# Kernel tuning notes

Measured on AMD Instinct MI355X. Metric: run time of the kernel, lower is better.

The kernel has to match this reference:

```python
import jax, jax.numpy as jnp
import numpy as np

B = 256
NE = 19          # electrodes (nodes per graph)
E = 60           # edges per graph
T = 25           # time samples averaged away
EPS = 1e-5


def _bn_channel(x, g, b, rm, rv):
    # x: (B, 19, F); BatchNorm1d over channel dim=1 (eval mode, running stats)
    inv = jax.lax.rsqrt(rv + EPS)
    return (x - rm[None, :, None]) * (g * inv)[None, :, None] + b[None, :, None]


def _bn_feat(x, g, b, rm, rv):
    # x: (N, F); BatchNorm1d over feature dim (eval mode)
    inv = jax.lax.rsqrt(rv + EPS)
    return (x - rm) * (g * inv) + b


def _graph_conv(x, src, dst, ew_rep, w_rel, b_rel, w_root, n_nodes):
    # PyG GraphConv: out_i = W_rel @ sum_{j->i} e_ji * x_j + b_rel + W_root @ x_i
    msg = x[src] * ew_rep[:, None]                         # gather + scale
    agg = jax.ops.segment_sum(msg, dst, num_segments=n_nodes)  # scatter-add
    return agg @ w_rel.T + b_rel + x @ w_root.T


def setup_inputs() -> dict:
    key = jax.random.key(0)
    ks = jax.random.split(key, 24)
    rng = np.random.RandomState(0)
    # base graph: 60 directed edges among 19 nodes
    base = rng.randint(0, NE, size=(2, E)).astype(np.int64)
    offs = (np.arange(B, dtype=np.int64) * NE)[None, :, None]  # (1,B,1)
    ei = (base[:, None, :] + offs).reshape(2, B * E)
    inp = {
        "x": jax.random.normal(ks[0], (B * NE, 40 * 20 * T), dtype=jnp.float32),
        "edge_index": jnp.asarray(ei),
        "batch": jnp.repeat(jnp.arange(B, dtype=jnp.int64), NE),
        "lin2_w": jax.random.normal(ks[1], (256, 800), jnp.float32) * 0.02,
        "lin2_b": jnp.zeros((256,), jnp.float32),
        "bn3_g": jnp.ones((NE,), jnp.float32), "bn3_b": jnp.zeros((NE,), jnp.float32),
        "bn3_rm": jnp.zeros((NE,), jnp.float32), "bn3_rv": jnp.ones((NE,), jnp.float32),
        "lin3_w": jax.random.normal(ks[2], (128, 256), jnp.float32) * 0.02,
        "lin3_b": jnp.zeros((128,), jnp.float32),
        "bn4_g": jnp.ones((NE,), jnp.float32), "bn4_b": jnp.zeros((NE,), jnp.float32),
        "bn4_rm": jnp.zeros((NE,), jnp.float32), "bn4_rv": jnp.ones((NE,), jnp.float32),
        "lin4_w": jax.random.normal(ks[3], (64, 128), jnp.float32) * 0.02,
        "lin4_b": jnp.zeros((64,), jnp.float32),
        "bn5_g": jnp.ones((NE,), jnp.float32), "bn5_b": jnp.zeros((NE,), jnp.float32),
        "bn5_rm": jnp.zeros((NE,), jnp.float32), "bn5_rv": jnp.ones((NE,), jnp.float32),
        "ew1": jnp.ones((E,), jnp.float32),
        "gc1_wrel": jax.random.normal(ks[4], (32, 64), jnp.float32) * 0.1,
        "gc1_brel": jnp.zeros((32,), jnp.float32),
        "gc1_wroot": jax.random.normal(ks[5], (32, 64), jnp.float32) * 0.1,
        "bn6_g": jnp.ones((32,), jnp.float32), "bn6_b": jnp.zeros((32,), jnp.float32),
        "bn6_rm": jnp.zeros((32,), jnp.float32), "bn6_rv": jnp.ones((32,), jnp.float32),
        "ew2": jnp.ones((E,), jnp.float32),
        "gc2_wrel": jax.random.normal(ks[6], (32, 32), jnp.float32) * 0.1,
        "gc2_brel": jnp.zeros((32,), jnp.float32),
        "gc2_wroot": jax.random.normal(ks[7], (32, 32), jnp.float32) * 0.1,
        "bn7_g": jnp.ones((32,), jnp.float32), "bn7_b": jnp.zeros((32,), jnp.float32),
        "bn7_rm": jnp.zeros((32,), jnp.float32), "bn7_rv": jnp.ones((32,), jnp.float32),
        "lin5_w": jax.random.normal(ks[8], (32, 32), jnp.float32) * 0.1,
        "lin5_b": jnp.zeros((32,), jnp.float32),
        "hm_w": jax.random.normal(ks[9], (3, 32), jnp.float32) * 0.1,
        "hm_b": jnp.zeros((3,), jnp.float32),
        "hb_w": jax.random.normal(ks[10], (2, 32), jnp.float32) * 0.1,
        "hb_b": jnp.zeros((2,), jnp.float32),
        "hd_w": jax.random.normal(ks[11], (2, 32), jnp.float32) * 0.1,
        "hd_b": jnp.zeros((2,), jnp.float32),
    }
    return inp


def reference(x, edge_index, batch,
              lin2_w, lin2_b, bn3_g, bn3_b, bn3_rm, bn3_rv,
              lin3_w, lin3_b, bn4_g, bn4_b, bn4_rm, bn4_rv,
              lin4_w, lin4_b, bn5_g, bn5_b, bn5_rm, bn5_rv,
              ew1, gc1_wrel, gc1_brel, gc1_wroot, bn6_g, bn6_b, bn6_rm, bn6_rv,
              ew2, gc2_wrel, gc2_brel, gc2_wroot, bn7_g, bn7_b, bn7_rm, bn7_rv,
              lin5_w, lin5_b, hm_w, hm_b, hb_w, hb_b, hd_w, hd_b):
    n_nodes = x.shape[0]
    b = n_nodes // NE
    # time-average CWT: (B,19,40,20,T) -> (B,19,800)
    h = x.reshape(b, NE, 40, 20, -1).mean(axis=4).reshape(b, NE, 800)
    # dense encoder (dropout = identity in eval)
    h = _bn_channel(jax.nn.relu(h @ lin2_w.T + lin2_b), bn3_g, bn3_b, bn3_rm, bn3_rv)
    h = _bn_channel(jax.nn.relu(h @ lin3_w.T + lin3_b), bn4_g, bn4_b, bn4_rm, bn4_rv)
    h = _bn_channel(jax.nn.relu(h @ lin4_w.T + lin4_b), bn5_g, bn5_b, bn5_rm, bn5_rv)
    h = h.reshape(n_nodes, 64)
    src, dst = edge_index[0], edge_index[1]
    ew1_rep = jnp.tile(ew1, b)
    ew2_rep = jnp.tile(ew2, b)
    h = _graph_conv(h, src, dst, ew1_rep, gc1_wrel, gc1_brel, gc1_wroot, n_nodes)
    h = _bn_feat(jax.nn.relu(h), bn6_g, bn6_b, bn6_rm, bn6_rv)
    h = _graph_conv(h, src, dst, ew2_rep, gc2_wrel, gc2_brel, gc2_wroot, n_nodes)
    h = _bn_feat(jax.nn.relu(h), bn7_g, bn7_b, bn7_rm, bn7_rv)
    # global max pool over nodes of each graph
    z = jax.ops.segment_max(h, batch, num_segments=b)
    z = jax.nn.relu(z @ lin5_w.T + lin5_b)
    return (z @ hm_w.T + hm_b, z @ hb_w.T + hb_b, z @ hd_w.T + hd_b)
```

## Files before the change

kernel.cpp:

```cpp
#include <hip/hip_runtime.h>
#include <math.h>

#define EPSBN 1e-5f

__global__ __launch_bounds__(256)
void mean25_kernel(const float* __restrict__ x, float* __restrict__ h1)
{
    __shared__ __align__(16) float s[6400];
    const int t = threadIdx.x;
    const float4* xv = (const float4*)(x + (size_t)blockIdx.x * 6400);
    float4* sv = (float4*)s;
#pragma unroll
    for (int i = 0; i < 6; ++i) sv[i * 256 + t] = xv[i * 256 + t];
    if (t < 64) sv[1536 + t] = xv[1536 + t];
    __syncthreads();
    const float* p = s + t * 25;
    float acc = 0.f;
#pragma unroll
    for (int k = 0; k < 25; ++k) acc += p[k];
    h1[(size_t)blockIdx.x * 256 + t] = acc * (1.0f / 25.0f);
}

__global__ __launch_bounds__(256)
void sgemm_relu_bnch(const float* __restrict__ A, const float* __restrict__ W,
                     const float* __restrict__ bias,
                     const float* __restrict__ bg, const float* __restrict__ bb,
                     const float* __restrict__ brm, const float* __restrict__ brv,
                     float* __restrict__ C, int M, int N, int K)
{
    __shared__ __align__(16) float As[32][68];
    __shared__ __align__(16) float Ws[32][68];
    const int tid = threadIdx.x;
    const int bm = blockIdx.y * 64;
    const int bn = blockIdx.x * 64;
    const int tm0 = (tid >> 4) * 4;
    const int tn0 = (tid & 15) * 4;
    const int r0 = tid >> 3;
    const int c0 = (tid & 7) * 4;

    float acc[4][4] = {};
    const float* A0 = A + (size_t)(bm + r0) * K + c0;
    const float* A1 = A + (size_t)(bm + r0 + 32) * K + c0;
    const float* W0 = W + (size_t)(bn + r0) * K + c0;
    const float* W1 = W + (size_t)(bn + r0 + 32) * K + c0;

    float4 a0 = *(const float4*)A0;
    float4 a1 = *(const float4*)A1;
    float4 w0 = *(const float4*)W0;
    float4 w1 = *(const float4*)W1;

    for (int k0 = 0; k0 < K; k0 += 32) {
        __syncthreads();
        As[c0 + 0][r0] = a0.x; As[c0 + 1][r0] = a0.y;
        As[c0 + 2][r0] = a0.z; As[c0 + 3][r0] = a0.w;
        As[c0 + 0][r0 + 32] = a1.x; As[c0 + 1][r0 + 32] = a1.y;
        As[c0 + 2][r0 + 32] = a1.z; As[c0 + 3][r0 + 32] = a1.w;
        Ws[c0 + 0][r0] = w0.x; Ws[c0 + 1][r0] = w0.y;
        Ws[c0 + 2][r0] = w0.z; Ws[c0 + 3][r0] = w0.w;
        Ws[c0 + 0][r0 + 32] = w1.x; Ws[c0 + 1][r0 + 32] = w1.y;
        Ws[c0 + 2][r0 + 32] = w1.z; Ws[c0 + 3][r0 + 32] = w1.w;
        __syncthreads();
        if (k0 + 32 < K) {
            a0 = *(const float4*)(A0 + k0 + 32);
            a1 = *(const float4*)(A1 + k0 + 32);
            w0 = *(const float4*)(W0 + k0 + 32);
            w1 = *(const float4*)(W1 + k0 + 32);
        }
#pragma unroll
        for (int kk = 0; kk < 32; ++kk) {
            float4 a = *(const float4*)&As[kk][tm0];
            float4 b = *(const float4*)&Ws[kk][tn0];
            acc[0][0] += a.x * b.x; acc[0][1] += a.x * b.y;
            acc[0][2] += a.x * b.z; acc[0][3] += a.x * b.w;
            acc[1][0] += a.y * b.x; acc[1][1] += a.y * b.y;
            acc[1][2] += a.y * b.z; acc[1][3] += a.y * b.w;
            acc[2][0] += a.z * b.x; acc[2][1] += a.z * b.y;
            acc[2][2] += a.z * b.z; acc[2][3] += a.z * b.w;
            acc[3][0] += a.w * b.x; acc[3][1] += a.w * b.y;
            acc[3][2] += a.w * b.z; acc[3][3] += a.w * b.w;
        }
    }

    const float b0 = bias[bn + tn0 + 0];
    const float b1 = bias[bn + tn0 + 1];
    const float b2 = bias[bn + tn0 + 2];
    const float b3 = bias[bn + tn0 + 3];
#pragma unroll
    for (int i = 0; i < 4; ++i) {
        const int row = bm + tm0 + i;
        const int e = row % 19;
        const float scale = bg[e] * (1.0f / sqrtf(brv[e] + EPSBN));
        const float shift = bb[e] - brm[e] * scale;
        float4 o;
        o.x = fmaxf(acc[i][0] + b0, 0.f) * scale + shift;
        o.y = fmaxf(acc[i][1] + b1, 0.f) * scale + shift;
        o.z = fmaxf(acc[i][2] + b2, 0.f) * scale + shift;
        o.w = fmaxf(acc[i][3] + b3, 0.f) * scale + shift;
        *(float4*)(C + (size_t)row * N + bn + tn0) = o;
    }
}

__global__ __launch_bounds__(256)
void gemm23_fused(const float* __restrict__ h2,
                  const float* __restrict__ w3, const float* __restrict__ b3,
                  const float* __restrict__ g4, const float* __restrict__ bb4,
                  const float* __restrict__ rm4, const float* __restrict__ rv4,
                  const float* __restrict__ w4, const float* __restrict__ b4,
                  const float* __restrict__ g5, const float* __restrict__ bb5,
                  const float* __restrict__ rm5, const float* __restrict__ rv5,
                  float* __restrict__ h4out)
{
    __shared__ __align__(16) float As[32][36];
    __shared__ __align__(16) float Ws[32][132];
    __shared__ __align__(16) float C1[32][132];
    __shared__ __align__(16) float W4T[128][68];

    const int t = threadIdx.x;
    const int bm = blockIdx.x * 32;

    const int tm0 = (t >> 5) * 4;
    const int tn0 = (t & 31) * 4;
    const int ar = t >> 3;
    const int ac = (t & 7) * 4;

    float acc[4][4] = {};
    const float* Ap = h2 + (size_t)(bm + ar) * 256 + ac;
    float4 areg = *(const float4*)Ap;
    float4 wreg[4];
#pragma unroll
    for (int i = 0; i < 4; ++i)
        wreg[i] = *(const float4*)(w3 + (size_t)(ar + i * 32) * 256 + ac);

    for (int k0 = 0; k0 < 256; k0 += 32) {
        __syncthreads();
        As[ac + 0][ar] = areg.x; As[ac + 1][ar] = areg.y;
        As[ac + 2][ar] = areg.z; As[ac + 3][ar] = areg.w;
#pragma unroll
        for (int i = 0; i < 4; ++i) {
            const int row = ar + i * 32;
            Ws[ac + 0][row] = wreg[i].x; Ws[ac + 1][row] = wreg[i].y;
            Ws[ac + 2][row] = wreg[i].z; Ws[ac + 3][row] = wreg[i].w;
        }
        __syncthreads();
        if (k0 + 32 < 256) {
            areg = *(const float4*)(Ap + k0 + 32);
#pragma unroll
            for (int i = 0; i < 4; ++i)
                wreg[i] = *(const float4*)(w3 + (size_t)(ar + i * 32) * 256 + ac + k0 + 32);
        }
#pragma unroll
        for (int kk = 0; kk < 32; ++kk) {
            float4 a = *(const float4*)&As[kk][tm0];
            float4 b = *(const float4*)&Ws[kk][tn0];
            acc[0][0] += a.x * b.x; acc[0][1] += a.x * b.y;
            acc[0][2] += a.x * b.z; acc[0][3] += a.x * b.w;
            acc[1][0] += a.y * b.x; acc[1][1] += a.y * b.y;
            acc[1][2] += a.y * b.z; acc[1][3] += a.y * b.w;
            acc[2][0] += a.z * b.x; acc[2][1] += a.z * b.y;
            acc[2][2] += a.z * b.z; acc[2][3] += a.z * b.w;
            acc[3][0] += a.w * b.x; acc[3][1] += a.w * b.y;
            acc[3][2] += a.w * b.z; acc[3][3] += a.w * b.w;
        }
    }

    {
        const float c0 = b3[tn0 + 0], c1 = b3[tn0 + 1];
        const float c2 = b3[tn0 + 2], c3 = b3[tn0 + 3];
#pragma unroll
        for (int i = 0; i < 4; ++i) {
            const int e = (bm + tm0 + i) % 19;
            const float scale = g4[e] * (1.0f / sqrtf(rv4[e] + EPSBN));
            const float shift = bb4[e] - rm4[e] * scale;
            float4 o;
            o.x = fmaxf(acc[i][0] + c0, 0.f) * scale + shift;
            o.y = fmaxf(acc[i][1] + c1, 0.f) * scale + shift;
            o.z = fmaxf(acc[i][2] + c2, 0.f) * scale + shift;
            o.w = fmaxf(acc[i][3] + c3, 0.f) * scale + shift;
            *(float4*)&C1[tm0 + i][tn0] = o;
        }
    }

    {
        const int ln = t & 63;
        const int wq = t >> 6;
#pragma unroll
        for (int ii = 0; ii < 8; ++ii) {
            const int c4 = wq + ii * 4;
            float4 v = *(const float4*)(w4 + (size_t)ln * 128 + c4 * 4);
            W4T[c4 * 4 + 0][ln] = v.x;
            W4T[c4 * 4 + 1][ln] = v.y;
            W4T[c4 * 4 + 2][ln] = v.z;
            W4T[c4 * 4 + 3][ln] = v.w;
        }
    }
    __syncthreads();

    const int rm2 = (t >> 4) * 2;
    const int cn2 = (t & 15) * 4;
    float acc2[2][4] = {};
#pragma unroll 4
    for (int k = 0; k < 128; ++k) {
        const float a0 = C1[rm2 + 0][k];
        const float a1 = C1[rm2 + 1][k];
        const float4 w = *(const float4*)&W4T[k][cn2];
        acc2[0][0] += a0 * w.x; acc2[0][1] += a0 * w.y;
        acc2[0][2] += a0 * w.z; acc2[0][3] += a0 * w.w;
        acc2[1][0] += a1 * w.x; acc2[1][1] += a1 * w.y;
        acc2[1][2] += a1 * w.z; acc2[1][3] += a1 * w.w;
    }
    {
        const float c0 = b4[cn2 + 0], c1 = b4[cn2 + 1];
        const float c2 = b4[cn2 + 2], c3 = b4[cn2 + 3];
#pragma unroll
        for (int i = 0; i < 2; ++i) {
            const int row = bm + rm2 + i;
            const int e = row % 19;
            const float scale = g5[e] * (1.0f / sqrtf(rv5[e] + EPSBN));
            const float shift = bb5[e] - rm5[e] * scale;
            float4 o;
            o.x = fmaxf(acc2[i][0] + c0, 0.f) * scale + shift;
            o.y = fmaxf(acc2[i][1] + c1, 0.f) * scale + shift;
            o.z = fmaxf(acc2[i][2] + c2, 0.f) * scale + shift;
            o.w = fmaxf(acc2[i][3] + c3, 0.f) * scale + shift;
            *(float4*)(h4out + (size_t)row * 64 + cn2) = o;
        }
    }
}

__global__ __launch_bounds__(128)
void graph_head_kernel(const float* __restrict__ h,
                       const int* __restrict__ ei,
                       const float* __restrict__ ew1, const float* __restrict__ ew2,
                       const float* __restrict__ wrel1, const float* __restrict__ brel1,
                       const float* __restrict__ wroot1,
                       const float* __restrict__ g6, const float* __restrict__ b6,
                       const float* __restrict__ rm6, const float* __restrict__ rv6,
                       const float* __restrict__ wrel2, const float* __restrict__ brel2,
                       const float* __restrict__ wroot2,
                       const float* __restrict__ g7, const float* __restrict__ b7,
                       const float* __restrict__ rm7, const float* __restrict__ rv7,
                       const float* __restrict__ lin5w, const float* __restrict__ lin5b,
                       const float* __restrict__ hmw, const float* __restrict__ hmb,
                       const float* __restrict__ hbw, const float* __restrict__ hbb,
                       const float* __restrict__ hdw, const float* __restrict__ hdb,
                       float* __restrict__ out, int nB, int nEdgeTot)
{
    __shared__ __align__(16) float sh[19 * 64];
    __shared__ __align__(16) float sagg[19 * 64];
    __shared__ __align__(16) float sh2[19 * 32];
    __shared__ __align__(16) float sagg2[19 * 32];
    __shared__ __align__(16) float sh3[19 * 32];
    __shared__ __align__(16) float swrel1[32 * 64];
    __shared__ __align__(16) float swroot1[32 * 64];
    __shared__ __align__(16) float swrel2[32 * 32];
    __shared__ __align__(16) float swroot2[32 * 32];
    __shared__ __align__(16) float slin5[32 * 32];
    __shared__ float sz[32], szz[32];
    __shared__ int ssrc[60], sdst[60];
    __shared__ float sew1[60], sew2[60];

    const int t = threadIdx.x;
    const int g = blockIdx.x;

    for (int i = t; i < 19 * 64; i += 128) { sh[i] = h[(size_t)g * 19 * 64 + i]; sagg[i] = 0.f; }
    for (int i = t; i < 19 * 32; i += 128) sagg2[i] = 0.f;
    for (int i = t; i < 2048; i += 128) { swrel1[i] = wrel1[i]; swroot1[i] = wroot1[i]; }
    for (int i = t; i < 1024; i += 128) { swrel2[i] = wrel2[i]; swroot2[i] = wroot2[i]; slin5[i] = lin5w[i]; }
    if (t < 60) {
        ssrc[t] = ei[g * 60 + t] - g * 19;
        sdst[t] = ei[nEdgeTot + g * 60 + t] - g * 19;
        sew1[t] = ew1[t];
        sew2[t] = ew2[t];
    }
    __syncthreads();

    if (t < 64) {
        for (int e = 0; e < 60; ++e)
            sagg[sdst[e] * 64 + t] += sew1[e] * sh[ssrc[e] * 64 + t];
    }
    __syncthreads();

    for (int idx = t; idx < 19 * 32; idx += 128) {
        const int n = idx >> 5, j = idx & 31;
        const float4* ag = (const float4*)&sagg[n * 64];
        const float4* hg = (const float4*)&sh[n * 64];
        const float4* wr = (const float4*)&swrel1[j * 64];
        const float4* wo = (const float4*)&swroot1[j * 64];
        float acc = brel1[j];
#pragma unroll
        for (int k = 0; k < 16; ++k) {
            float4 a = ag[k], w = wr[k], x = hg[k], u = wo[k];
            acc += a.x * w.x + a.y * w.y + a.z * w.z + a.w * w.w;
            acc += x.x * u.x + x.y * u.y + x.z * u.z + x.w * u.w;
        }
        float v = fmaxf(acc, 0.f);
        const float scale = g6[j] * (1.0f / sqrtf(rv6[j] + EPSBN));
        sh2[idx] = (v - rm6[j]) * scale + b6[j];
    }
    __syncthreads();

    if (t < 32) {
        for (int e = 0; e < 60; ++e)
            sagg2[sdst[e] * 32 + t] += sew2[e] * sh2[ssrc[e] * 32 + t];
    }
    __syncthreads();

    for (int idx = t; idx < 19 * 32; idx += 128) {
        const int n = idx >> 5, j = idx & 31;
        const float4* ag = (const float4*)&sagg2[n * 32];
        const float4* hg = (const float4*)&sh2[n * 32];
        const float4* wr = (const float4*)&swrel2[j * 32];
        const float4* wo = (const float4*)&swroot2[j * 32];
        float acc = brel2[j];
#pragma unroll
        for (int k = 0; k < 8; ++k) {
            float4 a = ag[k], w = wr[k], x = hg[k], u = wo[k];
            acc += a.x * w.x + a.y * w.y + a.z * w.z + a.w * w.w;
            acc += x.x * u.x + x.y * u.y + x.z * u.z + x.w * u.w;
        }
        float v = fmaxf(acc, 0.f);
        const float scale = g7[j] * (1.0f / sqrtf(rv7[j] + EPSBN));
        sh3[idx] = (v - rm7[j]) * scale + b7[j];
    }
    __syncthreads();

    if (t < 32) {
        float m = sh3[t];
        for (int n = 1; n < 19; ++n) m = fmaxf(m, sh3[n * 32 + t]);
        sz[t] = m;
    }
    __syncthreads();

    if (t < 32) {
        float acc = lin5b[t];
        const float4* zp = (const float4*)sz;
        const float4* wp = (const float4*)&slin5[t * 32];
#pragma unroll
        for (int k = 0; k < 8; ++k) {
            float4 z = zp[k], w = wp[k];
            acc += z.x * w.x + z.y * w.y + z.z * w.z + z.w * w.w;
        }
        szz[t] = fmaxf(acc, 0.f);
    }
    __syncthreads();

    if (t < 3) {
        float acc = hmb[t];
        for (int k = 0; k < 32; ++k) acc += szz[k] * hmw[t * 32 + k];
        out[g * 3 + t] = acc;
    } else if (t < 5) {
        const int j = t - 3;
        float acc = hbb[j];
        for (int k = 0; k < 32; ++k) acc += szz[k] * hbw[j * 32 + k];
        out[nB * 3 + g * 2 + j] = acc;
    } else if (t < 7) {
        const int j = t - 5;
        float acc = hdb[j];
        for (int k = 0; k < 32; ++k) acc += szz[k] * hdw[j * 32 + k];
        out[nB * 5 + g * 2 + j] = acc;
    }
}

extern "C" void kernel_launch(void* const* d_in, const int* in_sizes, int n_in,
                              void* d_out, int out_size, void* d_ws, size_t ws_size,
                              hipStream_t stream)
{
    const float* x       = (const float*)d_in[0];
    const int*   ei      = (const int*)d_in[1];
    const float* lin2_w  = (const float*)d_in[3];
    const float* lin2_b  = (const float*)d_in[4];
    const float* bn3_g   = (const float*)d_in[5];
    const float* bn3_b   = (const float*)d_in[6];
    const float* bn3_rm  = (const float*)d_in[7];
    const float* bn3_rv  = (const float*)d_in[8];
    const float* lin3_w  = (const float*)d_in[9];
    const float* lin3_b  = (const float*)d_in[10];
    const float* bn4_g   = (const float*)d_in[11];
    const float* bn4_b   = (const float*)d_in[12];
    const float* bn4_rm  = (const float*)d_in[13];
    const float* bn4_rv  = (const float*)d_in[14];
    const float* lin4_w  = (const float*)d_in[15];
    const float* lin4_b  = (const float*)d_in[16];
    const float* bn5_g   = (const float*)d_in[17];
    const float* bn5_b   = (const float*)d_in[18];
    const float* bn5_rm  = (const float*)d_in[19];
    const float* bn5_rv  = (const float*)d_in[20];
    const float* ew1     = (const float*)d_in[21];
    const float* gc1_wrel  = (const float*)d_in[22];
    const float* gc1_brel  = (const float*)d_in[23];
    const float* gc1_wroot = (const float*)d_in[24];
    const float* bn6_g   = (const float*)d_in[25];
    const float* bn6_b   = (const float*)d_in[26];
    const float* bn6_rm  = (const float*)d_in[27];
    const float* bn6_rv  = (const float*)d_in[28];
    const float* ew2     = (const float*)d_in[29];
    const float* gc2_wrel  = (const float*)d_in[30];
    const float* gc2_brel  = (const float*)d_in[31];
    const float* gc2_wroot = (const float*)d_in[32];
    const float* bn7_g   = (const float*)d_in[33];
    const float* bn7_b   = (const float*)d_in[34];
    const float* bn7_rm  = (const float*)d_in[35];
    const float* bn7_rv  = (const float*)d_in[36];
    const float* lin5_w  = (const float*)d_in[37];
    const float* lin5_b  = (const float*)d_in[38];
    const float* hm_w    = (const float*)d_in[39];
    const float* hm_b    = (const float*)d_in[40];
    const float* hb_w    = (const float*)d_in[41];
    const float* hb_b    = (const float*)d_in[42];
    const float* hd_w    = (const float*)d_in[43];
    const float* hd_b    = (const float*)d_in[44];

    const int n_nodes = in_sizes[0] / 20000;
    const int B = n_nodes / 19;

    float* h1 = (float*)d_ws;
    float* h2 = h1 + (size_t)n_nodes * 800;
    float* h4 = h2 + (size_t)n_nodes * 256;

    mean25_kernel<<<(n_nodes * 800) / 256, 256, 0, stream>>>(x, h1);

    dim3 g1(256 / 64, n_nodes / 64);
    sgemm_relu_bnch<<<g1, 256, 0, stream>>>(h1, lin2_w, lin2_b,
                                            bn3_g, bn3_b, bn3_rm, bn3_rv,
                                            h2, n_nodes, 256, 800);

    gemm23_fused<<<n_nodes / 32, 256, 0, stream>>>(h2,
                                                   lin3_w, lin3_b,
                                                   bn4_g, bn4_b, bn4_rm, bn4_rv,
                                                   lin4_w, lin4_b,
                                                   bn5_g, bn5_b, bn5_rm, bn5_rv,
                                                   h4);

    graph_head_kernel<<<B, 128, 0, stream>>>(h4, ei, ew1, ew2,
                                             gc1_wrel, gc1_brel, gc1_wroot,
                                             bn6_g, bn6_b, bn6_rm, bn6_rv,
                                             gc2_wrel, gc2_brel, gc2_wroot,
                                             bn7_g, bn7_b, bn7_rm, bn7_rv,
                                             lin5_w, lin5_b,
                                             hm_w, hm_b, hb_w, hb_b, hd_w, hd_b,
                                             (float*)d_out, B, B * 60);
}
```

Before: 693.1 us.

## Fuse lin3/lin4 dense layers into per-graph graph head kernel

Merges the lin3+lin4 GEMM kernel and the graph-conv/head kernel into one kernel with one block per graph, computing the 19-node dense layers in shared memory. This removes a launch and the global write/read of the intermediate h4 activations. In exchange, every block re-streams the lin3 weight matrix from cache, and the grid is limited to one block per graph.

```diff
diff --git a/kernel.cpp b/kernel.cpp
--- a/kernel.cpp
+++ b/kernel.cpp
@@ -101,160 +101,44 @@
 }
 
 __global__ __launch_bounds__(256)
-void gemm23_fused(const float* __restrict__ h2,
-                  const float* __restrict__ w3, const float* __restrict__ b3,
-                  const float* __restrict__ g4, const float* __restrict__ bb4,
-                  const float* __restrict__ rm4, const float* __restrict__ rv4,
-                  const float* __restrict__ w4, const float* __restrict__ b4,
-                  const float* __restrict__ g5, const float* __restrict__ bb5,
-                  const float* __restrict__ rm5, const float* __restrict__ rv5,
-                  float* __restrict__ h4out)
+void tail_fused(const float* __restrict__ h2,
+                const int* __restrict__ ei,
+                const float* __restrict__ w3, const float* __restrict__ b3,
+                const float* __restrict__ g4, const float* __restrict__ bb4,
+                const float* __restrict__ rm4, const float* __restrict__ rv4,
+                const float* __restrict__ w4, const float* __restrict__ b4,
+                const float* __restrict__ g5, const float* __restrict__ bb5,
+                const float* __restrict__ rm5, const float* __restrict__ rv5,
+                const float* __restrict__ ew1, const float* __restrict__ ew2,
+                const float* __restrict__ wrel1, const float* __restrict__ brel1,
+                const float* __restrict__ wroot1,
+                const float* __restrict__ g6, const float* __restrict__ b6,
+                const float* __restrict__ rm6, const float* __restrict__ rv6,
+                const float* __restrict__ wrel2, const float* __restrict__ brel2,
+                const float* __restrict__ wroot2,
+                const float* __restrict__ g7, const float* __restrict__ b7,
+                const float* __restrict__ rm7, const float* __restrict__ rv7,
+                const float* __restrict__ lin5w, const float* __restrict__ lin5b,
+                const float* __restrict__ hmw, const float* __restrict__ hmb,
+                const float* __restrict__ hbw, const float* __restrict__ hbb,
+                const float* __restrict__ hdw, const float* __restrict__ hdb,
+                float* __restrict__ out, int nB, int nEdgeTot)
 {
-    __shared__ __align__(16) float As[32][36];
-    __shared__ __align__(16) float Ws[32][132];
-    __shared__ __align__(16) float C1[32][132];
+    __shared__ __align__(16) float sH2[20][260];
+    __shared__ __align__(16) float w3c[128][36];
+    __shared__ __align__(16) float C1[20][132];
     __shared__ __align__(16) float W4T[128][68];
-
-    const int t = threadIdx.x;
-    const int bm = blockIdx.x * 32;
-
-    const int tm0 = (t >> 5) * 4;
-    const int tn0 = (t & 31) * 4;
-    const int ar = t >> 3;
-    const int ac = (t & 7) * 4;
-
-    float acc[4][4] = {};
-    const float* Ap = h2 + (size_t)(bm + ar) * 256 + ac;
-    float4 areg = *(const float4*)Ap;
-    float4 wreg[4];
-#pragma unroll
-    for (int i = 0; i < 4; ++i)
-        wreg[i] = *(const float4*)(w3 + (size_t)(ar + i * 32) * 256 + ac);
-
-    for (int k0 = 0; k0 < 256; k0 += 32) {
-        __syncthreads();
-        As[ac + 0][ar] = areg.x; As[ac + 1][ar] = areg.y;
-        As[ac + 2][ar] = areg.z; As[ac + 3][ar] = areg.w;
-#pragma unroll
-        for (int i = 0; i < 4; ++i) {
-            const int row = ar + i * 32;
-            Ws[ac + 0][row] = wreg[i].x; Ws[ac + 1][row] = wreg[i].y;
-            Ws[ac + 2][row] = wreg[i].z; Ws[ac + 3][row] = wreg[i].w;
-        }
-        __syncthreads();
-        if (k0 + 32 < 256) {
-            areg = *(const float4*)(Ap + k0 + 32);
-#pragma unroll
-            for (int i = 0; i < 4; ++i)
-                wreg[i] = *(const float4*)(w3 + (size_t)(ar + i * 32) * 256 + ac + k0 + 32);
-        }
-#pragma unroll
-        for (int kk = 0; kk < 32; ++kk) {
-            float4 a = *(const float4*)&As[kk][tm0];
-            float4 b = *(const float4*)&Ws[kk][tn0];
-            acc[0][0] += a.x * b.x; acc[0][1] += a.x * b.y;
-            acc[0][2] += a.x * b.z; acc[0][3] += a.x * b.w;
-            acc[1][0] += a.y * b.x; acc[1][1] += a.y * b.y;
-            acc[1][2] += a.y * b.z; acc[1][3] += a.y * b.w;
-            acc[2][0] += a.z * b.x; acc[2][1] += a.z * b.y;
-            acc[2][2] += a.z * b.z; acc[2][3] += a.z * b.w;
-            acc[3][0] += a.w * b.x; acc[3][1] += a.w * b.y;
-            acc[3][2] += a.w * b.z; acc[3][3] += a.w * b.w;
-        }
-    }
-
-    {
-        const float c0 = b3[tn0 + 0], c1 = b3[tn0 + 1];
-        const float c2 = b3[tn0 + 2], c3 = b3[tn0 + 3];
-#pragma unroll
-        for (int i = 0; i < 4; ++i) {
-            const int e = (bm + tm0 + i) % 19;
-            const float scale = g4[e] * (1.0f / sqrtf(rv4[e] + EPSBN));
-            const float shift = bb4[e] - rm4[e] * scale;
-            float4 o;
-            o.x = fmaxf(acc[i][0] + c0, 0.f) * scale + shift;
-            o.y = fmaxf(acc[i][1] + c1, 0.f) * scale + shift;
-            o.z = fmaxf(acc[i][2] + c2, 0.f) * scale + shift;
-            o.w = fmaxf(acc[i][3] + c3, 0.f) * scale + shift;
-            *(float4*)&C1[tm0 + i][tn0] = o;
-        }
-    }
-
-    {
-        const int ln = t & 63;
-        const int wq = t >> 6;
-#pragma unroll
-        for (int ii = 0; ii < 8; ++ii) {
-            const int c4 = wq + ii * 4;
-            float4 v = *(const float4*)(w4 + (size_t)ln * 128 + c4 * 4);
-            W4T[c4 * 4 + 0][ln] = v.x;
-            W4T[c4 * 4 + 1][ln] = v.y;
-            W4T[c4 * 4 + 2][ln] = v.z;
-            W4T[c4 * 4 + 3][ln] = v.w;
-        }
-    }
-    __syncthreads();
-
-    const int rm2 = (t >> 4) * 2;
-    const int cn2 = (t & 15) * 4;
-    float acc2[2][4] = {};
-#pragma unroll 4
-    for (int k = 0; k < 128; ++k) {
-        const float a0 = C1[rm2 + 0][k];
-        const float a1 = C1[rm2 + 1][k];
-        const float4 w = *(const float4*)&W4T[k][cn2];
-        acc2[0][0] += a0 * w.x; acc2[0][1] += a0 * w.y;
-        acc2[0][2] += a0 * w.z; acc2[0][3] += a0 * w.w;
-        acc2[1][0] += a1 * w.x; acc2[1][1] += a1 * w.y;
-        acc2[1][2] += a1 * w.z; acc2[1][3] += a1 * w.w;
-    }
-    {
-        const float c0 = b4[cn2 + 0], c1 = b4[cn2 + 1];
-        const float c2 = b4[cn2 + 2], c3 = b4[cn2 + 3];
-#pragma unroll
-        for (int i = 0; i < 2; ++i) {
-            const int row = bm + rm2 + i;
-            const int e = row % 19;
-            const float scale = g5[e] * (1.0f / sqrtf(rv5[e] + EPSBN));
-            const float shift = bb5[e] - rm5[e] * scale;
-            float4 o;
-            o.x = fmaxf(acc2[i][0] + c0, 0.f) * scale + shift;
-            o.y = fmaxf(acc2[i][1] + c1, 0.f) * scale + shift;
-            o.z = fmaxf(acc2[i][2] + c2, 0.f) * scale + shift;
-            o.w = fmaxf(acc2[i][3] + c3, 0.f) * scale + shift;
-            *(float4*)(h4out + (size_t)row * 64 + cn2) = o;
-        }
-    }
-}
-
-__global__ __launch_bounds__(128)
-void graph_head_kernel(const float* __restrict__ h,
-                       const int* __restrict__ ei,
-                       const float* __restrict__ ew1, const float* __restrict__ ew2,
-                       const float* __restrict__ wrel1, const float* __restrict__ brel1,
-                       const float* __restrict__ wroot1,
-                       const float* __restrict__ g6, const float* __restrict__ b6,
-                       const float* __restrict__ rm6, const float* __restrict__ rv6,
-                       const float* __restrict__ wrel2, const float* __restrict__ brel2,
-                       const float* __restrict__ wroot2,
-                       const float* __restrict__ g7, const float* __restrict__ b7,
-                       const float* __restrict__ rm7, const float* __restrict__ rv7,
-                       const float* __restrict__ lin5w, const float* __restrict__ lin5b,
-                       const float* __restrict__ hmw, const float* __restrict__ hmb,
-                       const float* __restrict__ hbw, const float* __restrict__ hbb,
-                       const float* __restrict__ hdw, const float* __restrict__ hdb,
-                       float* __restrict__ out, int nB, int nEdgeTot)
-{
-    __shared__ __align__(16) float sh[19 * 64];
-    __shared__ __align__(16) float sagg[19 * 64];
-    __shared__ __align__(16) float sh2[19 * 32];
+    __shared__ __align__(16) float sh4[20][68];
+    __shared__ __align__(16) float sagg[19][68];
+    __shared__ __align__(16) float sh2g[19 * 32];
     __shared__ __align__(16) float sagg2[19 * 32];
     __shared__ __align__(16) float sh3[19 * 32];
-    __shared__ __align__(16) float swrel1[32 * 64];
-    __shared__ __align__(16) float swroot1[32 * 64];
-    __shared__ __align__(16) float swrel2[32 * 32];
-    __shared__ __align__(16) float swroot2[32 * 32];
-    __shared__ __align__(16) float slin5[32 * 32];
+    __shared__ __align__(16) float swrel1[2048];
+    __shared__ __align__(16) float swroot1[2048];
+    __shared__ __align__(16) float swrel2[1024];
+    __shared__ __align__(16) float swroot2[1024];
+    __shared__ __align__(16) float slin5[1024];
+    __shared__ float s4s[19], s4h[19], s5s[19], s5h[19];
     __shared__ float sz[32], szz[32];
     __shared__ int ssrc[60], sdst[60];
     __shared__ float sew1[60], sew2[60];
@@ -262,28 +146,124 @@
     const int t = threadIdx.x;
     const int g = blockIdx.x;
 
-    for (int i = t; i < 19 * 64; i += 128) { sh[i] = h[(size_t)g * 19 * 64 + i]; sagg[i] = 0.f; }
-    for (int i = t; i < 19 * 32; i += 128) sagg2[i] = 0.f;
-    for (int i = t; i < 2048; i += 128) { swrel1[i] = wrel1[i]; swroot1[i] = wroot1[i]; }
-    for (int i = t; i < 1024; i += 128) { swrel2[i] = wrel2[i]; swroot2[i] = wroot2[i]; slin5[i] = lin5w[i]; }
+    {
+        const float4* src = (const float4*)(h2 + (size_t)g * 19 * 256);
+        for (int f = t; f < 1216; f += 256) {
+            const int row = f >> 6, c4 = f & 63;
+            *((float4*)&sH2[row][c4 * 4]) = src[f];
+        }
+        if (t < 65) *((float4*)&sH2[19][t * 4]) = make_float4(0.f, 0.f, 0.f, 0.f);
+    }
+    for (int i = t; i < 2048; i += 256) { swrel1[i] = wrel1[i]; swroot1[i] = wroot1[i]; }
+    for (int i = t; i < 1024; i += 256) { swrel2[i] = wrel2[i]; swroot2[i] = wroot2[i]; slin5[i] = lin5w[i]; }
+    for (int i = t; i < 19 * 68; i += 256) ((float*)sagg)[i] = 0.f;
+    for (int i = t; i < 19 * 32; i += 256) sagg2[i] = 0.f;
     if (t < 60) {
         ssrc[t] = ei[g * 60 + t] - g * 19;
         sdst[t] = ei[nEdgeTot + g * 60 + t] - g * 19;
         sew1[t] = ew1[t];
         sew2[t] = ew2[t];
+    } else if (t >= 64 && t < 83) {
+        const int e = t - 64;
+        const float sc = g4[e] * (1.0f / sqrtf(rv4[e] + EPSBN));
+        s4s[e] = sc; s4h[e] = bb4[e] - rm4[e] * sc;
+    } else if (t >= 96 && t < 115) {
+        const int e = t - 96;
+        const float sc = g5[e] * (1.0f / sqrtf(rv5[e] + EPSBN));
+        s5s[e] = sc; s5h[e] = bb5[e] - rm5[e] * sc;
+    }
+
+    const int n1 = t >> 1;
+    const int mh = (t & 1) * 10;
+    const int wn = t >> 3;
+    const int wk = (t & 7) * 4;
+    float acc1[10] = {};
+    float4 wpre[4];
+#pragma unroll
+    for (int i = 0; i < 4; ++i)
+        wpre[i] = *(const float4*)(w3 + (size_t)(wn + 32 * i) * 256 + wk);
+
+    for (int kc = 0; kc < 8; ++kc) {
+        const int k0 = kc * 32;
+        __syncthreads();
+#pragma unroll
+        for (int i = 0; i < 4; ++i)
+            *((float4*)&w3c[wn + 32 * i][wk]) = wpre[i];
+        __syncthreads();
+        if (kc < 7) {
+#pragma unroll
+            for (int i = 0; i < 4; ++i)
+                wpre[i] = *(const float4*)(w3 + (size_t)(wn + 32 * i) * 256 + wk + k0 + 32);
+        }
+#pragma unroll
+        for (int k4 = 0; k4 < 8; ++k4) {
+            const float4 w = *(const float4*)&w3c[n1][k4 * 4];
+#pragma unroll
+            for (int r = 0; r < 10; ++r) {
+                const float4 a = *(const float4*)&sH2[mh + r][k0 + k4 * 4];
+                acc1[r] += a.x * w.x + a.y * w.y + a.z * w.z + a.w * w.w;
+            }
+        }
+    }
+    {
+        const float bn = b3[n1];
+#pragma unroll
+        for (int r = 0; r < 10; ++r) {
+            const int row = mh + r;
+            const int e = (row < 19) ? row : 0;
+            C1[row][n1] = fmaxf(acc1[r] + bn, 0.f) * s4s[e] + s4h[e];
+        }
+    }
+
+    {
+        const int ln = t & 63, wq = t >> 6;
+#pragma unroll
+        for (int ii = 0; ii < 8; ++ii) {
+            const int c4 = wq + ii * 4;
+            const float4 v = *(const float4*)(w4 + (size_t)ln * 128 + c4 * 4);
+            W4T[c4 * 4 + 0][ln] = v.x;
+            W4T[c4 * 4 + 1][ln] = v.y;
+            W4T[c4 * 4 + 2][ln] = v.z;
+            W4T[c4 * 4 + 3][ln] = v.w;
+        }
+    }
+    __syncthreads();
+
+    const int n2 = t & 63;
+    const int mq = (t >> 6) * 5;
+    float acc2[5] = {};
+    for (int k4 = 0; k4 < 32; ++k4) {
+        const float ww0 = W4T[k4 * 4 + 0][n2];
+        const float ww1 = W4T[k4 * 4 + 1][n2];
+        const float ww2 = W4T[k4 * 4 + 2][n2];
+        const float ww3 = W4T[k4 * 4 + 3][n2];
+#pragma unroll
+        for (int r = 0; r < 5; ++r) {
+            const float4 a = *(const float4*)&C1[mq + r][k4 * 4];
+            acc2[r] += a.x * ww0 + a.y * ww1 + a.z * ww2 + a.w * ww3;
+        }
+    }
+    {
+        const float bn = b4[n2];
+#pragma unroll
+        for (int r = 0; r < 5; ++r) {
+            const int row = mq + r;
+            const int e = (row < 19) ? row : 0;
+            sh4[row][n2] = fmaxf(acc2[r] + bn, 0.f) * s5s[e] + s5h[e];
+        }
     }
     __syncthreads();
 
     if (t < 64) {
         for (int e = 0; e < 60; ++e)
-            sagg[sdst[e] * 64 + t] += sew1[e] * sh[ssrc[e] * 64 + t];
-    }
-    __syncthreads();
-
-    for (int idx = t; idx < 19 * 32; idx += 128) {
+            sagg[sdst[e]][t] += sew1[e] * sh4[ssrc[e]][t];
+    }
+    __syncthreads();
+
+    for (int idx = t; idx < 19 * 32; idx += 256) {
         const int n = idx >> 5, j = idx & 31;
-        const float4* ag = (const float4*)&sagg[n * 64];
-        const float4* hg = (const float4*)&sh[n * 64];
+        const float4* ag = (const float4*)&sagg[n][0];
+        const float4* hg = (const float4*)&sh4[n][0];
         const float4* wr = (const float4*)&swrel1[j * 64];
         const float4* wo = (const float4*)&swroot1[j * 64];
         float acc = brel1[j];
@@ -295,20 +275,20 @@
         }
         float v = fmaxf(acc, 0.f);
         const float scale = g6[j] * (1.0f / sqrtf(rv6[j] + EPSBN));
-        sh2[idx] = (v - rm6[j]) * scale + b6[j];
+        sh2g[idx] = (v - rm6[j]) * scale + b6[j];
     }
     __syncthreads();
 
     if (t < 32) {
         for (int e = 0; e < 60; ++e)
-            sagg2[sdst[e] * 32 + t] += sew2[e] * sh2[ssrc[e] * 32 + t];
-    }
-    __syncthreads();
-
-    for (int idx = t; idx < 19 * 32; idx += 128) {
+            sagg2[sdst[e] * 32 + t] += sew2[e] * sh2g[ssrc[e] * 32 + t];
+    }
+    __syncthreads();
+
+    for (int idx = t; idx < 19 * 32; idx += 256) {
         const int n = idx >> 5, j = idx & 31;
         const float4* ag = (const float4*)&sagg2[n * 32];
-        const float4* hg = (const float4*)&sh2[n * 32];
+        const float4* hg = (const float4*)&sh2g[n * 32];
         const float4* wr = (const float4*)&swrel2[j * 32];
         const float4* wo = (const float4*)&swroot2[j * 32];
         float acc = brel2[j];
@@ -415,7 +395,6 @@
 
     float* h1 = (float*)d_ws;
     float* h2 = h1 + (size_t)n_nodes * 800;
-    float* h4 = h2 + (size_t)n_nodes * 256;
 
     mean25_kernel<<<(n_nodes * 800) / 256, 256, 0, stream>>>(x, h1);
 
@@ -424,19 +403,17 @@
                                             bn3_g, bn3_b, bn3_rm, bn3_rv,
                                             h2, n_nodes, 256, 800);
 
-    gemm23_fused<<<n_nodes / 32, 256, 0, stream>>>(h2,
-                                                   lin3_w, lin3_b,
-                                                   bn4_g, bn4_b, bn4_rm, bn4_rv,
-                                                   lin4_w, lin4_b,
-                                                   bn5_g, bn5_b, bn5_rm, bn5_rv,
-                                                   h4);
-
-    graph_head_kernel<<<B, 128, 0, stream>>>(h4, ei, ew1, ew2,
-                                             gc1_wrel, gc1_brel, gc1_wroot,
-                                             bn6_g, bn6_b, bn6_rm, bn6_rv,
-                                             gc2_wrel, gc2_brel, gc2_wroot,
-                                             bn7_g, bn7_b, bn7_rm, bn7_rv,
-                                             lin5_w, lin5_b,
-                                             hm_w, hm_b, hb_w, hb_b, hd_w, hd_b,
-                                             (float*)d_out, B, B * 60);
+    tail_fused<<<B, 256, 0, stream>>>(h2, ei,
+                                      lin3_w, lin3_b,
+                                      bn4_g, bn4_b, bn4_rm, bn4_rv,
+                                      lin4_w, lin4_b,
+                                      bn5_g, bn5_b, bn5_rm, bn5_rv,
+                                      ew1, ew2,
+                                      gc1_wrel, gc1_brel, gc1_wroot,
+                                      bn6_g, bn6_b, bn6_rm, bn6_rv,
+                                      gc2_wrel, gc2_brel, gc2_wroot,
+                                      bn7_g, bn7_b, bn7_rm, bn7_rv,
+                                      lin5_w, lin5_b,
+                                      hm_w, hm_b, hb_w, hb_b, hd_w, hd_b,
+                                      (float*)d_out, B, B * 60);
 }
```

Measured after the change: 713.9 us. 1.03x slower.

## Fuse time-mean reduction into first dense layer GEMM per graph

Applied to the files above, without the earlier changes.

Replaces the separate time-averaging kernel and the first tiled SGEMM with a single kernel that has one block per graph. The block streams the 19 node rows of x in K-chunks through double-buffered shared memory, averages them on the fly, and accumulates the lin2 product with bias, ReLU and channel BatchNorm in the epilogue. This removes the h1 intermediate round-trip to global memory and one launch. It limits the grid to one block per graph, with large shared memory use, which may reduce memory-level parallelism on the dominant x stream.

```diff
diff --git a/kernel.cpp b/kernel.cpp
--- a/kernel.cpp
+++ b/kernel.cpp
@@ -4,99 +4,122 @@
 #define EPSBN 1e-5f
 
 __global__ __launch_bounds__(256)
-void mean25_kernel(const float* __restrict__ x, float* __restrict__ h1)
+void front_fused(const float* __restrict__ x,
+                 const float* __restrict__ w2, const float* __restrict__ b2,
+                 const float* __restrict__ g3, const float* __restrict__ bb3,
+                 const float* __restrict__ rm3, const float* __restrict__ rv3,
+                 float* __restrict__ h2)
 {
-    __shared__ __align__(16) float s[6400];
+    __shared__ __align__(16) float sx[2][19 * 400];
+    __shared__ __align__(16) float sw[2][16 * 264];
+    __shared__ __align__(16) float At[20 * 16];
+    __shared__ float s3s[19], s3h[19];
+
     const int t = threadIdx.x;
-    const float4* xv = (const float4*)(x + (size_t)blockIdx.x * 6400);
-    float4* sv = (float4*)s;
-#pragma unroll
-    for (int i = 0; i < 6; ++i) sv[i * 256 + t] = xv[i * 256 + t];
-    if (t < 64) sv[1536 + t] = xv[1536 + t];
-    __syncthreads();
-    const float* p = s + t * 25;
-    float acc = 0.f;
-#pragma unroll
-    for (int k = 0; k < 25; ++k) acc += p[k];
-    h1[(size_t)blockIdx.x * 256 + t] = acc * (1.0f / 25.0f);
-}
-
-__global__ __launch_bounds__(256)
-void sgemm_relu_bnch(const float* __restrict__ A, const float* __restrict__ W,
-                     const float* __restrict__ bias,
-                     const float* __restrict__ bg, const float* __restrict__ bb,
-                     const float* __restrict__ brm, const float* __restrict__ brv,
-                     float* __restrict__ C, int M, int N, int K)
-{
-    __shared__ __align__(16) float As[32][68];
-    __shared__ __align__(16) float Ws[32][68];
-    const int tid = threadIdx.x;
-    const int bm = blockIdx.y * 64;
-    const int bn = blockIdx.x * 64;
-    const int tm0 = (tid >> 4) * 4;
-    const int tn0 = (tid & 15) * 4;
-    const int r0 = tid >> 3;
-    const int c0 = (tid & 7) * 4;
-
-    float acc[4][4] = {};
-    const float* A0 = A + (size_t)(bm + r0) * K + c0;
-    const float* A1 = A + (size_t)(bm + r0 + 32) * K + c0;
-    const float* W0 = W + (size_t)(bn + r0) * K + c0;
-    const float* W1 = W + (size_t)(bn + r0 + 32) * K + c0;
-
-    float4 a0 = *(const float4*)A0;
-    float4 a1 = *(const float4*)A1;
-    float4 w0 = *(const float4*)W0;
-    float4 w1 = *(const float4*)W1;
-
-    for (int k0 = 0; k0 < K; k0 += 32) {
+    const int g = blockIdx.x;
+
+    int xoff[8];
+    size_t xbase[8];
+#pragma unroll
+    for (int i = 0; i < 8; ++i) {
+        const int f = t + 256 * i;
+        int r = f / 100;
+        const int c4 = f - r * 100;
+        if (r > 18) r = 18;
+        xoff[i] = r * 400 + c4 * 4;
+        xbase[i] = (size_t)(g * 19 + r) * 20000 + (size_t)c4 * 4;
+    }
+    const bool x7ok = (t < 108);
+    const int wq = t & 3;
+    int wn[4];
+#pragma unroll
+    for (int i = 0; i < 4; ++i) wn[i] = (t >> 2) + 64 * i;
+
+    if (t < 19) {
+        const float sc = g3[t] * (1.0f / sqrtf(rv3[t] + EPSBN));
+        s3s[t] = sc; s3h[t] = bb3[t] - rm3[t] * sc;
+    }
+
+    float4 xv[8], wv[4];
+    float acc[19];
+#pragma unroll
+    for (int r = 0; r < 19; ++r) acc[r] = 0.f;
+
+#pragma unroll
+    for (int i = 0; i < 7; ++i) xv[i] = *(const float4*)(x + xbase[i]);
+    if (x7ok) xv[7] = *(const float4*)(x + xbase[7]);
+#pragma unroll
+    for (int i = 0; i < 4; ++i) wv[i] = *(const float4*)(w2 + (size_t)wn[i] * 800 + wq * 4);
+#pragma unroll
+    for (int i = 0; i < 7; ++i) *(float4*)&sx[0][xoff[i]] = xv[i];
+    if (x7ok) *(float4*)&sx[0][xoff[7]] = xv[7];
+#pragma unroll
+    for (int i = 0; i < 4; ++i) {
+        sw[0][(wq * 4 + 0) * 264 + wn[i]] = wv[i].x;
+        sw[0][(wq * 4 + 1) * 264 + wn[i]] = wv[i].y;
+        sw[0][(wq * 4 + 2) * 264 + wn[i]] = wv[i].z;
+        sw[0][(wq * 4 + 3) * 264 + wn[i]] = wv[i].w;
+    }
+    __syncthreads();
+
+    int cur = 0;
+    for (int kc = 0; kc < 50; ++kc) {
+        if (kc < 49) {
+            const size_t xk = (size_t)(kc + 1) * 400;
+            const size_t wk = (size_t)(kc + 1) * 16;
+#pragma unroll
+            for (int i = 0; i < 7; ++i) xv[i] = *(const float4*)(x + xbase[i] + xk);
+            if (x7ok) xv[7] = *(const float4*)(x + xbase[7] + xk);
+#pragma unroll
+            for (int i = 0; i < 4; ++i)
+                wv[i] = *(const float4*)(w2 + (size_t)wn[i] * 800 + wk + wq * 4);
+        }
+
+        for (int idx = t; idx < 304; idx += 256) {
+            const int r = idx >> 4, kk = idx & 15;
+            const float* p = &sx[cur][r * 400 + kk * 25];
+            float s = 0.f;
+#pragma unroll
+            for (int j = 0; j < 25; ++j) s += p[j];
+            At[r * 16 + kk] = s * (1.0f / 25.0f);
+        }
         __syncthreads();
-        As[c0 + 0][r0] = a0.x; As[c0 + 1][r0] = a0.y;
-        As[c0 + 2][r0] = a0.z; As[c0 + 3][r0] = a0.w;
-        As[c0 + 0][r0 + 32] = a1.x; As[c0 + 1][r0 + 32] = a1.y;
-        As[c0 + 2][r0 + 32] = a1.z; As[c0 + 3][r0 + 32] = a1.w;
-        Ws[c0 + 0][r0] = w0.x; Ws[c0 + 1][r0] = w0.y;
-        Ws[c0 + 2][r0] = w0.z; Ws[c0 + 3][r0] = w0.w;
-        Ws[c0 + 0][r0 + 32] = w1.x; Ws[c0 + 1][r0 + 32] = w1.y;
-        Ws[c0 + 2][r0 + 32] = w1.z; Ws[c0 + 3][r0 + 32] = w1.w;
+
+#pragma unroll
+        for (int k4 = 0; k4 < 4; ++k4) {
+            const float w0 = sw[cur][(k4 * 4 + 0) * 264 + t];
+            const float w1 = sw[cur][(k4 * 4 + 1) * 264 + t];
+            const float w2v = sw[cur][(k4 * 4 + 2) * 264 + t];
+            const float w3v = sw[cur][(k4 * 4 + 3) * 264 + t];
+#pragma unroll
+            for (int r = 0; r < 19; ++r) {
+                const float4 a = *(const float4*)&At[r * 16 + k4 * 4];
+                acc[r] += a.x * w0 + a.y * w1 + a.z * w2v + a.w * w3v;
+            }
+        }
+
+        if (kc < 49) {
+            const int nxt = cur ^ 1;
+#pragma unroll
+            for (int i = 0; i < 7; ++i) *(float4*)&sx[nxt][xoff[i]] = xv[i];
+            if (x7ok) *(float4*)&sx[nxt][xoff[7]] = xv[7];
+#pragma unroll
+            for (int i = 0; i < 4; ++i) {
+                sw[nxt][(wq * 4 + 0) * 264 + wn[i]] = wv[i].x;
+                sw[nxt][(wq * 4 + 1) * 264 + wn[i]] = wv[i].y;
+                sw[nxt][(wq * 4 + 2) * 264 + wn[i]] = wv[i].z;
+                sw[nxt][(wq * 4 + 3) * 264 + wn[i]] = wv[i].w;
+            }
+        }
         __syncthreads();
-        if (k0 + 32 < K) {
-            a0 = *(const float4*)(A0 + k0 + 32);
-            a1 = *(const float4*)(A1 + k0 + 32);
-            w0 = *(const float4*)(W0 + k0 + 32);
-            w1 = *(const float4*)(W1 + k0 + 32);
-        }
-#pragma unroll
-        for (int kk = 0; kk < 32; ++kk) {
-            float4 a = *(const float4*)&As[kk][tm0];
-            float4 b = *(const float4*)&Ws[kk][tn0];
-            acc[0][0] += a.x * b.x; acc[0][1] += a.x * b.y;
-            acc[0][2] += a.x * b.z; acc[0][3] += a.x * b.w;
-            acc[1][0] += a.y * b.x; acc[1][1] += a.y * b.y;
-            acc[1][2] += a.y * b.z; acc[1][3] += a.y * b.w;
-            acc[2][0] += a.z * b.x; acc[2][1] += a.z * b.y;
-            acc[2][2] += a.z * b.z; acc[2][3] += a.z * b.w;
-            acc[3][0] += a.w * b.x; acc[3][1] += a.w * b.y;
-            acc[3][2] += a.w * b.z; acc[3][3] += a.w * b.w;
-        }
-    }
-
-    const float b0 = bias[bn + tn0 + 0];
-    const float b1 = bias[bn + tn0 + 1];
-    const float b2 = bias[bn + tn0 + 2];
-    const float b3 = bias[bn + tn0 + 3];
-#pragma unroll
-    for (int i = 0; i < 4; ++i) {
-        const int row = bm + tm0 + i;
-        const int e = row % 19;
-        const float scale = bg[e] * (1.0f / sqrtf(brv[e] + EPSBN));
-        const float shift = bb[e] - brm[e] * scale;
-        float4 o;
-        o.x = fmaxf(acc[i][0] + b0, 0.f) * scale + shift;
-        o.y = fmaxf(acc[i][1] + b1, 0.f) * scale + shift;
-        o.z = fmaxf(acc[i][2] + b2, 0.f) * scale + shift;
-        o.w = fmaxf(acc[i][3] + b3, 0.f) * scale + shift;
-        *(float4*)(C + (size_t)row * N + bn + tn0) = o;
+        cur ^= 1;
+    }
+
+    const float bn = b2[t];
+#pragma unroll
+    for (int r = 0; r < 19; ++r) {
+        const float v = fmaxf(acc[r] + bn, 0.f) * s3s[r] + s3h[r];
+        h2[((size_t)g * 19 + r) * 256 + t] = v;
     }
 }
 
@@ -181,12 +204,11 @@
     }
 
     {
-        const int ln = t & 63;
-        const int wq = t >> 6;
+        const int ln = t & 63, wq = t >> 6;
 #pragma unroll
         for (int ii = 0; ii < 8; ++ii) {
             const int c4 = wq + ii * 4;
-            float4 v = *(const float4*)(w4 + (size_t)ln * 128 + c4 * 4);
+            const float4 v = *(const float4*)(w4 + (size_t)ln * 128 + c4 * 4);
             W4T[c4 * 4 + 0][ln] = v.x;
             W4T[c4 * 4 + 1][ln] = v.y;
             W4T[c4 * 4 + 2][ln] = v.z;
@@ -413,16 +435,11 @@
     const int n_nodes = in_sizes[0] / 20000;
     const int B = n_nodes / 19;
 
-    float* h1 = (float*)d_ws;
-    float* h2 = h1 + (size_t)n_nodes * 800;
+    float* h2 = (float*)d_ws;
     float* h4 = h2 + (size_t)n_nodes * 256;
 
-    mean25_kernel<<<(n_nodes * 800) / 256, 256, 0, stream>>>(x, h1);
-
-    dim3 g1(256 / 64, n_nodes / 64);
-    sgemm_relu_bnch<<<g1, 256, 0, stream>>>(h1, lin2_w, lin2_b,
-                                            bn3_g, bn3_b, bn3_rm, bn3_rv,
-                                            h2, n_nodes, 256, 800);
+    front_fused<<<B, 256, 0, stream>>>(x, lin2_w, lin2_b,
+                                       bn3_g, bn3_b, bn3_rm, bn3_rv, h2);
 
     gemm23_fused<<<n_nodes / 32, 256, 0, stream>>>(h2,
                                                    lin3_w, lin3_b,
```

Measured after the change: 743.6 us. +7.3%, slower.
